# Optimization experiments

Hardware: AMD Instinct MI355X
Metric: run time of the kernel (lower is better)

The kernel has to match this reference:

```python
import jax, jax.numpy as jnp
import numpy as np

N = 512          # octave output grid resolution per cube side
M = 256          # input octave resolution
FACTOR = 0.5     # 2 ** (-factor), factor = 1
EPS = 1e-12


def make_cube_faces(n):
    # two triangles per quad on each of the 6 n x n side grids
    idx = np.arange(n * n).reshape(n, n)
    a = idx[:-1, :-1].ravel(); b = idx[:-1, 1:].ravel()
    c = idx[1:, :-1].ravel(); d = idx[1:, 1:].ravel()
    tris = np.concatenate([np.stack([a, b, c], 1), np.stack([b, d, c], 1)], 0)
    faces = np.concatenate([tris + s * n * n for s in range(6)], 0)
    return jnp.asarray(faces, jnp.int32)  # [F, 3]


def to_stacked(t):
    # [1, 6*m*m, 3] -> [6, 3, m, m]
    m = int(round((t.shape[1] // 6) ** 0.5))
    return t.reshape(6, m, m, 3).transpose(0, 3, 1, 2)


def to_vertices(s):
    # [6, 3, m, m] -> [1, 6*m*m, 3]
    return s.transpose(0, 2, 3, 1).reshape(1, -1, 3)


def resize_bilinear_ac(t, n):
    # bilinear, align_corners=True, square input [.., m, m] -> [.., n, n]
    m = t.shape[-1]
    coords = jnp.linspace(0.0, m - 1.0, n)
    i0 = jnp.clip(jnp.floor(coords).astype(jnp.int32), 0, m - 1)
    i1 = jnp.minimum(i0 + 1, m - 1)
    w = (coords - i0).astype(t.dtype)
    t = t[..., i0, :] * (1.0 - w)[:, None] + t[..., i1, :] * w[:, None]
    t = t[..., :, i0] * (1.0 - w) + t[..., :, i1] * w
    return t


def compute_face_normals(vert, faces):
    v = vert[0]                                  # [V, 3]
    v0, v1, v2 = v[faces[:, 0]], v[faces[:, 1]], v[faces[:, 2]]
    fn = jnp.cross(v1 - v0, v2 - v0)             # [F, 3]
    nrm = jnp.linalg.norm(fn, axis=-1, keepdims=True)
    return fn / jnp.maximum(nrm, EPS)


def compute_vertex_normals(vert, faces, face_normals):
    V = vert.shape[1]
    flat_idx = faces.reshape(-1)                          # [3F] f0v0,f0v1,f0v2,...
    rep = jnp.repeat(face_normals, 3, axis=0)             # [3F, 3]
    acc = jax.ops.segment_sum(rep, flat_idx, num_segments=V)  # scatter-add
    nrm = jnp.linalg.norm(acc, axis=-1, keepdims=True)
    return (acc / jnp.maximum(nrm, EPS))[None]            # [1, V, 3]


def get_vertex_normals(vert, faces):
    fn = compute_face_normals(vert, faces)
    normals = compute_vertex_normals(vert, faces, fn)
    stacked = to_stacked(normals)                         # [6, 3, n, n]
    sign = jnp.array([-1.0, 1.0, 1.0, -1.0, -1.0, 1.0], stacked.dtype)
    stacked = stacked * sign[:, None, None, None]
    return to_vertices(stacked)


def setup_inputs() -> dict:
    key = jax.random.key(0)
    k1, k2 = jax.random.split(key)
    vrt = jax.random.normal(k1, (1, 6 * M * M, 3), jnp.float32)
    nrm = jax.random.normal(k2, (1, 6 * M * M, 3), jnp.float32)
    ps = jnp.zeros((6, 1, N, N), jnp.float32)   # nn.Parameter(zeros * noise)
    faces = make_cube_faces(N)
    return {"vrt": vrt, "nrm": nrm, "ps": ps, "faces": faces}


def reference(vrt, nrm, ps, faces):
    vrt_s = resize_bilinear_ac(to_stacked(vrt), N)                 # [6,3,n,n]
    nrm_mag = jnp.linalg.norm(resize_bilinear_ac(to_stacked(nrm), N),
                              axis=1, keepdims=True)               # [6,1,n,n]
    stacked = vrt_s + FACTOR * jax.nn.sigmoid(ps) * nrm_mag
    vert = to_vertices(stacked)                                    # [1, V, 3]
    normals = get_vertex_normals(vert, faces)
    return vert, faces, normals
```

## Files before the change

### kernel.cpp

```cpp
#include <hip/hip_runtime.h>
#include <math.h>

#define NSZ 512
#define MSZ 256
#define NPIX (6 * NSZ * NSZ)
#define NQ   ((NSZ - 1) * (NSZ - 1))
#define NFACE (6 * 2 * NQ)
#define F3TOT (NFACE * 3)
#define TS 32
#define HS (TS + 2)
#define QS (TS + 1)
#define NVB (6 * 16 * 16)
#define NFT (F3TOT / 4)
#define NFB ((NFT + 255) / 256)

__device__ inline float fast_rcp(float x) {
    float r = __builtin_amdgcn_rcpf(x);
    return r * (2.0f - x * r);
}
__device__ inline float fast_rsqrt(float d) {
    float r = __builtin_amdgcn_rsqf(d);
    return r * (1.5f - 0.5f * d * r * r);
}
__device__ inline float fast_sigmoid(float x) {
    float e = __builtin_amdgcn_exp2f(-1.442695040888963f * x);
    return fast_rcp(1.0f + e);
}

__device__ inline void sample_vert(const float* __restrict__ vrt,
                                   const float* __restrict__ nrm,
                                   const float* __restrict__ ps,
                                   int f, int y, int x, float out[3]) {
    const float scale = 255.0f / 511.0f;
    float cy = (float)y * scale;
    float cx = (float)x * scale;
    int iy0 = (int)floorf(cy); iy0 = iy0 < 0 ? 0 : (iy0 > MSZ - 1 ? MSZ - 1 : iy0);
    int ix0 = (int)floorf(cx); ix0 = ix0 < 0 ? 0 : (ix0 > MSZ - 1 ? MSZ - 1 : ix0);
    int iy1 = min(iy0 + 1, MSZ - 1);
    int ix1 = min(ix0 + 1, MSZ - 1);
    float wy = cy - (float)iy0;
    float wx = cx - (float)ix0;
    float w00 = (1.0f - wy) * (1.0f - wx);
    float w01 = (1.0f - wy) * wx;
    float w10 = wy * (1.0f - wx);
    float w11 = wy * wx;

    int fb  = f * (MSZ * MSZ);
    int i00 = (fb + iy0 * MSZ + ix0) * 3;
    int i01 = (fb + iy0 * MSZ + ix1) * 3;
    int i10 = (fb + iy1 * MSZ + ix0) * 3;
    int i11 = (fb + iy1 * MSZ + ix1) * 3;

    float vs[3], ns[3];
#pragma unroll
    for (int c = 0; c < 3; ++c) {
        vs[c] = vrt[i00 + c] * w00 + vrt[i01 + c] * w01 +
                vrt[i10 + c] * w10 + vrt[i11 + c] * w11;
        ns[c] = nrm[i00 + c] * w00 + nrm[i01 + c] * w01 +
                nrm[i10 + c] * w10 + nrm[i11 + c] * w11;
    }
    float d2  = ns[0] * ns[0] + ns[1] * ns[1] + ns[2] * ns[2];
    float mag = __builtin_amdgcn_sqrtf(d2);
    float sig = fast_sigmoid(ps[f * (NSZ * NSZ) + y * NSZ + x]);
    float add = 0.5f * sig * mag;
    out[0] = vs[0] + add;
    out[1] = vs[1] + add;
    out[2] = vs[2] + add;
}

__global__ __launch_bounds__(256) void k_all(const float* __restrict__ vrt,
                                             const float* __restrict__ nrm,
                                             const float* __restrict__ ps,
                                             float* __restrict__ out0,
                                             float* __restrict__ out1_f4,
                                             float* __restrict__ out2) {
    __shared__ float sv[HS * HS * 3];
    __shared__ float tn0[QS * QS * 3];
    __shared__ float tn1[QS * QS * 3];

    int blk = blockIdx.x;

    if (blk >= NVB) {
        int t = (blk - NVB) * 256 + threadIdx.x;
        if (t >= NFT) return;
        int o = t * 4;
        float vals[4];
#pragma unroll
        for (int k = 0; k < 4; ++k) {
            unsigned idx = (unsigned)(o + k);
            unsigned ti  = idx / 3u;
            unsigned c   = idx - ti * 3u;
            unsigned s   = ti / (2u * NQ);
            unsigned r1  = ti - s * (2u * NQ);
            unsigned ty  = r1 / NQ;
            unsigned qi  = r1 - ty * NQ;
            unsigned R   = qi / (NSZ - 1);
            unsigned Q   = qi - R * (NSZ - 1);
            unsigned a   = s * (NSZ * NSZ) + R * NSZ + Q;
            unsigned sel;
            if (c == 0)      sel = ty ? 1u : 0u;
            else if (c == 1) sel = ty ? (NSZ + 1u) : 1u;
            else             sel = NSZ;
            vals[k] = (float)(a + sel);
        }
        ((float4*)out1_f4)[t] = make_float4(vals[0], vals[1], vals[2], vals[3]);
        return;
    }

    int f  = blk >> 8;
    int t  = blk & 255;
    int tr = (t >> 4) * TS;
    int tq = (t & 15) * TS;

    for (int p = threadIdx.x; p < HS * HS; p += 256) {
        int pr = p / HS, pq = p - pr * HS;
        int y = tr + pr - 1, x = tq + pq - 1;
        int yc = min(max(y, 0), NSZ - 1);
        int xc = min(max(x, 0), NSZ - 1);
        float val[3];
        sample_vert(vrt, nrm, ps, f, yc, xc, val);
        sv[p * 3 + 0] = val[0];
        sv[p * 3 + 1] = val[1];
        sv[p * 3 + 2] = val[2];
        if (pr >= 1 && pr <= TS && pq >= 1 && pq <= TS) {
            int gi = (f * (NSZ * NSZ) + y * NSZ + x) * 3;
            out0[gi + 0] = val[0];
            out0[gi + 1] = val[1];
            out0[gi + 2] = val[2];
        }
    }
    __syncthreads();

    for (int p = threadIdx.x; p < QS * QS; p += 256) {
        int Ri = p / QS, Qi = p - Ri * QS;
        bool valid = ((unsigned)(tr + Ri - 1) < (unsigned)(NSZ - 1)) &&
                     ((unsigned)(tq + Qi - 1) < (unsigned)(NSZ - 1));
        float msk = valid ? 1.0f : 0.0f;
        #define SVL(rr, qq, c) sv[(((rr) * HS) + (qq)) * 3 + (c)]
        float ax0 = SVL(Ri,   Qi,   0), ay0 = SVL(Ri,   Qi,   1), az0 = SVL(Ri,   Qi,   2);
        float bx  = SVL(Ri,   Qi+1, 0), by  = SVL(Ri,   Qi+1, 1), bz  = SVL(Ri,   Qi+1, 2);
        float cx  = SVL(Ri+1, Qi,   0), cy  = SVL(Ri+1, Qi,   1), cz  = SVL(Ri+1, Qi,   2);
        float dx  = SVL(Ri+1, Qi+1, 0), dy  = SVL(Ri+1, Qi+1, 1), dz  = SVL(Ri+1, Qi+1, 2);
        #undef SVL

        {
            float e1x = bx - ax0, e1y = by - ay0, e1z = bz - az0;
            float e2x = cx - ax0, e2y = cy - ay0, e2z = cz - az0;
            float nx = e1y * e2z - e1z * e2y;
            float ny = e1z * e2x - e1x * e2z;
            float nz = e1x * e2y - e1y * e2x;
            float d  = fmaxf(nx * nx + ny * ny + nz * nz, 1e-24f);
            float r  = fast_rsqrt(d) * msk;
            tn0[p * 3 + 0] = nx * r;
            tn0[p * 3 + 1] = ny * r;
            tn0[p * 3 + 2] = nz * r;
        }
        {
            float e1x = dx - bx, e1y = dy - by, e1z = dz - bz;
            float e2x = cx - bx, e2y = cy - by, e2z = cz - bz;
            float nx = e1y * e2z - e1z * e2y;
            float ny = e1z * e2x - e1x * e2z;
            float nz = e1x * e2y - e1y * e2x;
            float d  = fmaxf(nx * nx + ny * ny + nz * nz, 1e-24f);
            float r  = fast_rsqrt(d) * msk;
            tn1[p * 3 + 0] = nx * r;
            tn1[p * 3 + 1] = ny * r;
            tn1[p * 3 + 2] = nz * r;
        }
    }
    __syncthreads();

    float sg = (f == 1 || f == 2 || f == 5) ? 1.0f : -1.0f;
    for (int p = threadIdx.x; p < TS * TS; p += 256) {
        int r = p >> 5, q = p & 31;
        int q00 = ((r    ) * QS + (q    )) * 3;
        int q01 = ((r    ) * QS + (q + 1)) * 3;
        int q10 = ((r + 1) * QS + (q    )) * 3;
        int q11 = ((r + 1) * QS + (q + 1)) * 3;

        float ax = tn0[q11 + 0] + tn0[q10 + 0] + tn0[q01 + 0]
                 + tn1[q10 + 0] + tn1[q00 + 0] + tn1[q01 + 0];
        float ay = tn0[q11 + 1] + tn0[q10 + 1] + tn0[q01 + 1]
                 + tn1[q10 + 1] + tn1[q00 + 1] + tn1[q01 + 1];
        float az = tn0[q11 + 2] + tn0[q10 + 2] + tn0[q01 + 2]
                 + tn1[q10 + 2] + tn1[q00 + 2] + tn1[q01 + 2];

        float d  = fmaxf(ax * ax + ay * ay + az * az, 1e-24f);
        float rs = fast_rsqrt(d) * sg;
        int gi = (f * (NSZ * NSZ) + (tr + r) * NSZ + (tq + q)) * 3;
        out2[gi + 0] = ax * rs;
        out2[gi + 1] = ay * rs;
        out2[gi + 2] = az * rs;
    }
}

extern "C" void kernel_launch(void* const* d_in, const int* in_sizes, int n_in,
                              void* d_out, int out_size, void* d_ws, size_t ws_size,
                              hipStream_t stream) {
    const float* vrt = (const float*)d_in[0];
    const float* nrm = (const float*)d_in[1];
    const float* ps  = (const float*)d_in[2];

    float* out0 = (float*)d_out;
    float* out1 = out0 + (size_t)NPIX * 3;
    float* out2 = out1 + (size_t)NFACE * 3;

    k_all<<<NVB + NFB, 256, 0, stream>>>(vrt, nrm, ps, out0, out1, out2);
}
```

Before: 29.11 us.

## Stage input patch in LDS, recompute normals per vertex, interleave face-index blocks

Each vertex tile first loads its small source patch of vrt/nrm into shared memory as float4, so bilinear sampling reads LDS instead of making repeated global gathers. The separate face-normal stage and its barrier are removed: each vertex now recomputes its six adjacent triangle normals from the float4 vertex tile. Face-index threads write 12 values with three float4 stores, stepping the index incrementally instead of doing per-element divisions. Face-writer blocks are interleaved two per vertex block so both kinds of work are spread across the grid. The cost is about three times more cross-product work per vertex, and boundary masking now depends on clamped samples producing degenerate triangles.

```diff
diff --git a/kernel.cpp b/kernel.cpp
--- a/kernel.cpp
+++ b/kernel.cpp
@@ -9,10 +9,10 @@
 #define F3TOT (NFACE * 3)
 #define TS 32
 #define HS (TS + 2)
-#define QS (TS + 1)
+#define PS 20
 #define NVB (6 * 16 * 16)
-#define NFT (F3TOT / 4)
-#define NFB ((NFT + 255) / 256)
+#define NFT12 (F3TOT / 12)
+#define GRID (NVB * 3)
 
 __device__ inline float fast_rcp(float x) {
     float r = __builtin_amdgcn_rcpf(x);
@@ -27,145 +27,132 @@
     return fast_rcp(1.0f + e);
 }
 
-__device__ inline void sample_vert(const float* __restrict__ vrt,
-                                   const float* __restrict__ nrm,
-                                   const float* __restrict__ ps,
-                                   int f, int y, int x, float out[3]) {
-    const float scale = 255.0f / 511.0f;
-    float cy = (float)y * scale;
-    float cx = (float)x * scale;
-    int iy0 = (int)floorf(cy); iy0 = iy0 < 0 ? 0 : (iy0 > MSZ - 1 ? MSZ - 1 : iy0);
-    int ix0 = (int)floorf(cx); ix0 = ix0 < 0 ? 0 : (ix0 > MSZ - 1 ? MSZ - 1 : ix0);
-    int iy1 = min(iy0 + 1, MSZ - 1);
-    int ix1 = min(ix0 + 1, MSZ - 1);
-    float wy = cy - (float)iy0;
-    float wx = cx - (float)ix0;
-    float w00 = (1.0f - wy) * (1.0f - wx);
-    float w01 = (1.0f - wy) * wx;
-    float w10 = wy * (1.0f - wx);
-    float w11 = wy * wx;
-
-    int fb  = f * (MSZ * MSZ);
-    int i00 = (fb + iy0 * MSZ + ix0) * 3;
-    int i01 = (fb + iy0 * MSZ + ix1) * 3;
-    int i10 = (fb + iy1 * MSZ + ix0) * 3;
-    int i11 = (fb + iy1 * MSZ + ix1) * 3;
-
-    float vs[3], ns[3];
-#pragma unroll
-    for (int c = 0; c < 3; ++c) {
-        vs[c] = vrt[i00 + c] * w00 + vrt[i01 + c] * w01 +
-                vrt[i10 + c] * w10 + vrt[i11 + c] * w11;
-        ns[c] = nrm[i00 + c] * w00 + nrm[i01 + c] * w01 +
-                nrm[i10 + c] * w10 + nrm[i11 + c] * w11;
-    }
-    float d2  = ns[0] * ns[0] + ns[1] * ns[1] + ns[2] * ns[2];
-    float mag = __builtin_amdgcn_sqrtf(d2);
-    float sig = fast_sigmoid(ps[f * (NSZ * NSZ) + y * NSZ + x]);
-    float add = 0.5f * sig * mag;
-    out[0] = vs[0] + add;
-    out[1] = vs[1] + add;
-    out[2] = vs[2] + add;
+__device__ inline void tri_acc4(const float4 A, const float4 B, const float4 C,
+                                float& ax, float& ay, float& az) {
+    float e1x = B.x - A.x, e1y = B.y - A.y, e1z = B.z - A.z;
+    float e2x = C.x - A.x, e2y = C.y - A.y, e2z = C.z - A.z;
+    float nx = e1y * e2z - e1z * e2y;
+    float ny = e1z * e2x - e1x * e2z;
+    float nz = e1x * e2y - e1y * e2x;
+    float d  = fmaxf(nx * nx + ny * ny + nz * nz, 1e-24f);
+    float r  = fast_rsqrt(d);
+    ax += nx * r; ay += ny * r; az += nz * r;
 }
 
 __global__ __launch_bounds__(256) void k_all(const float* __restrict__ vrt,
                                              const float* __restrict__ nrm,
                                              const float* __restrict__ ps,
                                              float* __restrict__ out0,
-                                             float* __restrict__ out1_f4,
+                                             float* __restrict__ out1,
                                              float* __restrict__ out2) {
-    __shared__ float sv[HS * HS * 3];
-    __shared__ float tn0[QS * QS * 3];
-    __shared__ float tn1[QS * QS * 3];
-
-    int blk = blockIdx.x;
-
-    if (blk >= NVB) {
-        int t = (blk - NVB) * 256 + threadIdx.x;
-        if (t >= NFT) return;
-        int o = t * 4;
-        float vals[4];
+    __shared__ float4 spv[PS * PS];
+    __shared__ float4 spn[PS * PS];
+    __shared__ float4 sv4[HS * HS];
+
+    int blk    = blockIdx.x;
+    int triple = blk / 3;
+    int pos    = blk - triple * 3;
+
+    if (pos != 0) {
+        int t = (triple * 2 + (pos - 1)) * 256 + threadIdx.x;
+        if (t >= NFT12) return;
+        unsigned ti = 4u * (unsigned)t;
+        unsigned s  = ti / (2u * NQ);
+        unsigned r1 = ti - s * (2u * NQ);
+        unsigned ty = (r1 >= (unsigned)NQ) ? 1u : 0u;
+        unsigned qi = r1 - ty * (unsigned)NQ;
+        unsigned R  = qi / (NSZ - 1);
+        unsigned Q  = qi - R * (NSZ - 1);
+        unsigned sbase = s << 18;
+        float v[12];
 #pragma unroll
         for (int k = 0; k < 4; ++k) {
-            unsigned idx = (unsigned)(o + k);
-            unsigned ti  = idx / 3u;
-            unsigned c   = idx - ti * 3u;
-            unsigned s   = ti / (2u * NQ);
-            unsigned r1  = ti - s * (2u * NQ);
-            unsigned ty  = r1 / NQ;
-            unsigned qi  = r1 - ty * NQ;
-            unsigned R   = qi / (NSZ - 1);
-            unsigned Q   = qi - R * (NSZ - 1);
-            unsigned a   = s * (NSZ * NSZ) + R * NSZ + Q;
-            unsigned sel;
-            if (c == 0)      sel = ty ? 1u : 0u;
-            else if (c == 1) sel = ty ? (NSZ + 1u) : 1u;
-            else             sel = NSZ;
-            vals[k] = (float)(a + sel);
+            unsigned a = sbase + (R << 9) + Q;
+            v[3 * k + 0] = (float)(a + (ty ? 1u : 0u));
+            v[3 * k + 1] = (float)(a + (ty ? (unsigned)(NSZ + 1) : 1u));
+            v[3 * k + 2] = (float)(a + (unsigned)NSZ);
+            Q++;
+            if (Q == (unsigned)(NSZ - 1)) {
+                Q = 0u; R++;
+                if (R == (unsigned)(NSZ - 1)) {
+                    R = 0u; ty++;
+                    if (ty == 2u) { ty = 0u; sbase += (unsigned)(NSZ * NSZ); }
+                }
+            }
         }
-        ((float4*)out1_f4)[t] = make_float4(vals[0], vals[1], vals[2], vals[3]);
+        float4* o = (float4*)out1 + 3 * t;
+        o[0] = make_float4(v[0], v[1], v[2],  v[3]);
+        o[1] = make_float4(v[4], v[5], v[6],  v[7]);
+        o[2] = make_float4(v[8], v[9], v[10], v[11]);
         return;
     }
 
-    int f  = blk >> 8;
-    int t  = blk & 255;
-    int tr = (t >> 4) * TS;
-    int tq = (t & 15) * TS;
-
+    int f   = triple >> 8;
+    int tl  = triple & 255;
+    int tr  = (tl >> 4) * TS;
+    int tq  = (tl & 15) * TS;
+    int fbm = f * (MSZ * MSZ);
+    int fbn = f * (NSZ * NSZ);
+
+    int iy_base = max(0, ((tr - 1) * (MSZ - 1)) / (NSZ - 1));
+    int ix_base = max(0, ((tq - 1) * (MSZ - 1)) / (NSZ - 1));
+
+    for (int p = threadIdx.x; p < PS * PS; p += 256) {
+        int r = p / PS, c = p - r * PS;
+        int iy = min(iy_base + r, MSZ - 1);
+        int ix = min(ix_base + c, MSZ - 1);
+        int g  = (fbm + iy * MSZ + ix) * 3;
+        spv[p] = make_float4(vrt[g], vrt[g + 1], vrt[g + 2], 0.0f);
+        spn[p] = make_float4(nrm[g], nrm[g + 1], nrm[g + 2], 0.0f);
+    }
+    __syncthreads();
+
+    const float scale = 255.0f / 511.0f;
     for (int p = threadIdx.x; p < HS * HS; p += 256) {
         int pr = p / HS, pq = p - pr * HS;
         int y = tr + pr - 1, x = tq + pq - 1;
         int yc = min(max(y, 0), NSZ - 1);
         int xc = min(max(x, 0), NSZ - 1);
-        float val[3];
-        sample_vert(vrt, nrm, ps, f, yc, xc, val);
-        sv[p * 3 + 0] = val[0];
-        sv[p * 3 + 1] = val[1];
-        sv[p * 3 + 2] = val[2];
+
+        float cy = (float)yc * scale;
+        float cx = (float)xc * scale;
+        int iy0 = (int)floorf(cy); iy0 = iy0 < 0 ? 0 : (iy0 > MSZ - 1 ? MSZ - 1 : iy0);
+        int ix0 = (int)floorf(cx); ix0 = ix0 < 0 ? 0 : (ix0 > MSZ - 1 ? MSZ - 1 : ix0);
+        int iy1 = min(iy0 + 1, MSZ - 1);
+        int ix1 = min(ix0 + 1, MSZ - 1);
+        float wy = cy - (float)iy0;
+        float wx = cx - (float)ix0;
+        float w00 = (1.0f - wy) * (1.0f - wx);
+        float w01 = (1.0f - wy) * wx;
+        float w10 = wy * (1.0f - wx);
+        float w11 = wy * wx;
+
+        int l00 = (iy0 - iy_base) * PS + (ix0 - ix_base);
+        int l01 = (iy0 - iy_base) * PS + (ix1 - ix_base);
+        int l10 = (iy1 - iy_base) * PS + (ix0 - ix_base);
+        int l11 = (iy1 - iy_base) * PS + (ix1 - ix_base);
+
+        float4 a00 = spv[l00], a01 = spv[l01], a10 = spv[l10], a11 = spv[l11];
+        float4 b00 = spn[l00], b01 = spn[l01], b10 = spn[l10], b11 = spn[l11];
+
+        float vx = a00.x * w00 + a01.x * w01 + a10.x * w10 + a11.x * w11;
+        float vy = a00.y * w00 + a01.y * w01 + a10.y * w10 + a11.y * w11;
+        float vz = a00.z * w00 + a01.z * w01 + a10.z * w10 + a11.z * w11;
+        float nx = b00.x * w00 + b01.x * w01 + b10.x * w10 + b11.x * w11;
+        float ny = b00.y * w00 + b01.y * w01 + b10.y * w10 + b11.y * w11;
+        float nz = b00.z * w00 + b01.z * w01 + b10.z * w10 + b11.z * w11;
+
+        float mag = __builtin_amdgcn_sqrtf(nx * nx + ny * ny + nz * nz);
+        float sig = fast_sigmoid(ps[fbn + yc * NSZ + xc]);
+        float add = 0.5f * sig * mag;
+        float ox = vx + add, oy = vy + add, oz = vz + add;
+
+        sv4[p] = make_float4(ox, oy, oz, 0.0f);
         if (pr >= 1 && pr <= TS && pq >= 1 && pq <= TS) {
-            int gi = (f * (NSZ * NSZ) + y * NSZ + x) * 3;
-            out0[gi + 0] = val[0];
-            out0[gi + 1] = val[1];
-            out0[gi + 2] = val[2];
-        }
-    }
-    __syncthreads();
-
-    for (int p = threadIdx.x; p < QS * QS; p += 256) {
-        int Ri = p / QS, Qi = p - Ri * QS;
-        bool valid = ((unsigned)(tr + Ri - 1) < (unsigned)(NSZ - 1)) &&
-                     ((unsigned)(tq + Qi - 1) < (unsigned)(NSZ - 1));
-        float msk = valid ? 1.0f : 0.0f;
-        #define SVL(rr, qq, c) sv[(((rr) * HS) + (qq)) * 3 + (c)]
-        float ax0 = SVL(Ri,   Qi,   0), ay0 = SVL(Ri,   Qi,   1), az0 = SVL(Ri,   Qi,   2);
-        float bx  = SVL(Ri,   Qi+1, 0), by  = SVL(Ri,   Qi+1, 1), bz  = SVL(Ri,   Qi+1, 2);
-        float cx  = SVL(Ri+1, Qi,   0), cy  = SVL(Ri+1, Qi,   1), cz  = SVL(Ri+1, Qi,   2);
-        float dx  = SVL(Ri+1, Qi+1, 0), dy  = SVL(Ri+1, Qi+1, 1), dz  = SVL(Ri+1, Qi+1, 2);
-        #undef SVL
-
-        {
-            float e1x = bx - ax0, e1y = by - ay0, e1z = bz - az0;
-            float e2x = cx - ax0, e2y = cy - ay0, e2z = cz - az0;
-            float nx = e1y * e2z - e1z * e2y;
-            float ny = e1z * e2x - e1x * e2z;
-            float nz = e1x * e2y - e1y * e2x;
-            float d  = fmaxf(nx * nx + ny * ny + nz * nz, 1e-24f);
-            float r  = fast_rsqrt(d) * msk;
-            tn0[p * 3 + 0] = nx * r;
-            tn0[p * 3 + 1] = ny * r;
-            tn0[p * 3 + 2] = nz * r;
-        }
-        {
-            float e1x = dx - bx, e1y = dy - by, e1z = dz - bz;
-            float e2x = cx - bx, e2y = cy - by, e2z = cz - bz;
-            float nx = e1y * e2z - e1z * e2y;
-            float ny = e1z * e2x - e1x * e2z;
-            float nz = e1x * e2y - e1y * e2x;
-            float d  = fmaxf(nx * nx + ny * ny + nz * nz, 1e-24f);
-            float r  = fast_rsqrt(d) * msk;
-            tn1[p * 3 + 0] = nx * r;
-            tn1[p * 3 + 1] = ny * r;
-            tn1[p * 3 + 2] = nz * r;
+            int gi = (fbn + y * NSZ + x) * 3;
+            out0[gi + 0] = ox;
+            out0[gi + 1] = oy;
+            out0[gi + 2] = oz;
         }
     }
     __syncthreads();
@@ -173,21 +160,26 @@
     float sg = (f == 1 || f == 2 || f == 5) ? 1.0f : -1.0f;
     for (int p = threadIdx.x; p < TS * TS; p += 256) {
         int r = p >> 5, q = p & 31;
-        int q00 = ((r    ) * QS + (q    )) * 3;
-        int q01 = ((r    ) * QS + (q + 1)) * 3;
-        int q10 = ((r + 1) * QS + (q    )) * 3;
-        int q11 = ((r + 1) * QS + (q + 1)) * 3;
-
-        float ax = tn0[q11 + 0] + tn0[q10 + 0] + tn0[q01 + 0]
-                 + tn1[q10 + 0] + tn1[q00 + 0] + tn1[q01 + 0];
-        float ay = tn0[q11 + 1] + tn0[q10 + 1] + tn0[q01 + 1]
-                 + tn1[q10 + 1] + tn1[q00 + 1] + tn1[q01 + 1];
-        float az = tn0[q11 + 2] + tn0[q10 + 2] + tn0[q01 + 2]
-                 + tn1[q10 + 2] + tn1[q00 + 2] + tn1[q01 + 2];
+        int lc = (r + 1) * HS + (q + 1);
+        float4 C  = sv4[lc];
+        float4 W  = sv4[lc - 1];
+        float4 E  = sv4[lc + 1];
+        float4 Nn = sv4[lc - HS];
+        float4 S  = sv4[lc + HS];
+        float4 NE = sv4[lc - HS + 1];
+        float4 SW = sv4[lc + HS - 1];
+
+        float ax = 0.0f, ay = 0.0f, az = 0.0f;
+        tri_acc4(C,  E,  S,  ax, ay, az);
+        tri_acc4(W,  C,  SW, ax, ay, az);
+        tri_acc4(Nn, NE, C,  ax, ay, az);
+        tri_acc4(C,  S,  SW, ax, ay, az);
+        tri_acc4(Nn, C,  W,  ax, ay, az);
+        tri_acc4(NE, E,  C,  ax, ay, az);
 
         float d  = fmaxf(ax * ax + ay * ay + az * az, 1e-24f);
         float rs = fast_rsqrt(d) * sg;
-        int gi = (f * (NSZ * NSZ) + (tr + r) * NSZ + (tq + q)) * 3;
+        int gi = (fbn + (tr + r) * NSZ + (tq + q)) * 3;
         out2[gi + 0] = ax * rs;
         out2[gi + 1] = ay * rs;
         out2[gi + 2] = az * rs;
@@ -205,5 +197,5 @@
     float* out1 = out0 + (size_t)NPIX * 3;
     float* out2 = out1 + (size_t)NFACE * 3;
 
-    k_all<<<NVB + NFB, 256, 0, stream>>>(vrt, nrm, ps, out0, out1, out2);
-}
+    k_all<<<GRID, 256, 0, stream>>>(vrt, nrm, ps, out0, out1, out2);
+}
```

Result: slower. 32.27 us (+10.9%).
